# Kernel optimization log

Measured on AMD Instinct MI355X. Metric: run time of the kernel, lower is better.

The kernel has to match this reference:

```python
import jax, jax.numpy as jnp
import numpy as np

B, T, IN, H = 128, 128, 64, 512  # batch, seq_len, input_size, encoded_size==hidden_size


def _cell(x, h, c, Wih, Whh, bih, bhh):
    # PyTorch LSTM gate order: i, f, g, o
    g = x @ Wih.T + h @ Whh.T + bih + bhh
    i, f, gg, o = jnp.split(g, 4, axis=-1)
    c = jax.nn.sigmoid(f) * c + jax.nn.sigmoid(i) * jnp.tanh(gg)
    h = jax.nn.sigmoid(o) * jnp.tanh(c)
    return h, c


def _lstm_layer(xs, Wih, Whh, bih, bhh):
    # xs: [T, B, din] -> ys: [T, B, H], zero initial state (as in the torch module)
    b = xs.shape[1]
    hdim = Whh.shape[1]
    h0 = jnp.zeros((b, hdim), xs.dtype)
    c0 = jnp.zeros((b, hdim), xs.dtype)

    def step(carry, x):
        h, c = _cell(x, carry[0], carry[1], Wih, Whh, bih, bhh)
        return (h, c), h

    _, ys = jax.lax.scan(step, (h0, c0), xs)
    return ys


def setup_inputs() -> dict:
    key = jax.random.key(0)
    ks = jax.random.split(key, 18)
    s = 1.0 / np.sqrt(H)  # torch LSTM default init scale
    r = lambda k, shp: jax.random.uniform(k, shp, jnp.float32, -s, s)
    return {
        "x": jax.random.normal(ks[0], (B, T, IN), jnp.float32),
        # encoder layer 0 (input IN) and layer 1 (input H)
        "eW_ih0": r(ks[1], (4 * H, IN)), "eW_hh0": r(ks[2], (4 * H, H)),
        "eb_ih0": r(ks[3], (4 * H,)), "eb_hh0": r(ks[4], (4 * H,)),
        "eW_ih1": r(ks[5], (4 * H, H)), "eW_hh1": r(ks[6], (4 * H, H)),
        "eb_ih1": r(ks[7], (4 * H,)), "eb_hh1": r(ks[8], (4 * H,)),
        # decoder layer 0 (input H = encoded_size) and layer 1
        "dW_ih0": r(ks[9], (4 * H, H)), "dW_hh0": r(ks[10], (4 * H, H)),
        "db_ih0": r(ks[11], (4 * H,)), "db_hh0": r(ks[12], (4 * H,)),
        "dW_ih1": r(ks[13], (4 * H, H)), "dW_hh1": r(ks[14], (4 * H, H)),
        "db_ih1": r(ks[15], (4 * H,)), "db_hh1": r(ks[16], (4 * H,)),
        # output projection
        "fc_W": r(ks[17], (IN, H)), "fc_b": jnp.zeros((IN,), jnp.float32),
    }


def reference(x, eW_ih0, eW_hh0, eb_ih0, eb_hh0, eW_ih1, eW_hh1, eb_ih1, eb_hh1,
              dW_ih0, dW_hh0, db_ih0, db_hh0, dW_ih1, dW_hh1, db_ih1, db_hh1,
              fc_W, fc_b):
    b, t = x.shape[0], x.shape[1]
    xs = jnp.swapaxes(x, 0, 1)  # [T, B, IN]
    # 2-layer encoder, take last timestep of top layer
    y0 = _lstm_layer(xs, eW_ih0, eW_hh0, eb_ih0, eb_hh0)
    y1 = _lstm_layer(y0, eW_ih1, eW_hh1, eb_ih1, eb_hh1)
    z = y1[-1]  # [B, H] constant decoder input each step
    hdim = dW_hh0.shape[1]
    zero = jnp.zeros((b, hdim), x.dtype)

    def step(carry, _):
        h0, c0, h1, c1 = carry
        h0, c0 = _cell(z, h0, c0, dW_ih0, dW_hh0, db_ih0, db_hh0)
        h1, c1 = _cell(h0, h1, c1, dW_ih1, dW_hh1, db_ih1, db_hh1)
        return (h0, c0, h1, c1), h1

    _, hs = jax.lax.scan(step, (zero, zero, zero, zero), None, length=t)  # [T, B, H]
    out = jnp.einsum('tbh,ih->tbi', hs, fc_W) + fc_b
    return jnp.swapaxes(out, 0, 1)  # [B, T, IN]
```

## Files before the change

### kernel.cpp

```cpp
#include <hip/hip_runtime.h>
#include <cstdint>

#define TT 128

typedef _Float16 f16;
typedef _Float16 f16x8 __attribute__((ext_vector_type(8)));
typedef float f32x4 __attribute__((ext_vector_type(4)));
typedef unsigned int u32;
typedef unsigned long long u64;

#define OFF_H0    16384
#define OFF_H1    (OFF_H0 + 262144)
#define OFF_D0    (OFF_H1 + 262144)
#define OFF_D1    (OFF_D0 + 262144)
#define OFF_XH    (OFF_D1 + 262144)
#define OFF_HS    (OFF_XH + 2097152)

#define L_SA   0
#define L_SB   24576
#define L_TOT  65536

#define MFMA16(a,b,c) __builtin_amdgcn_mfma_f32_16x16x32_f16((a),(b),(c),0,0,0)

__device__ __forceinline__ float sigm(float x){ return 1.f/(1.f+__expf(-x)); }
__device__ __forceinline__ float tanhft(float x){ return 1.f - 2.f/(__expf(2.f*x)+1.f); }

__device__ __forceinline__ f16x8 wfrag(const float* __restrict__ src, int K, int srow,
                                       int k, int j){
  const float* p = src + srow*K + (k<<5) + (j<<3);
  float4 v0 = *(const float4*)p;
  float4 v1 = *(const float4*)(p+4);
  f16x8 r;
  r[0]=(f16)v0.x; r[1]=(f16)v0.y; r[2]=(f16)v0.z; r[3]=(f16)v0.w;
  r[4]=(f16)v1.x; r[5]=(f16)v1.y; r[6]=(f16)v1.z; r[7]=(f16)v1.w;
  return r;
}

__device__ __forceinline__ void stage1(const char* R, char* S, int tid){
  const int cgs = tid >> 3, rr = (tid & 7) << 1;
  const char* gp = R + cgs*512 + rr*32;
  char* sp = S + cgs*768 + rr*48;
  u64 t0[8];
#pragma unroll
  for (int e = 0; e < 2; ++e)
#pragma unroll
    for (int i = 0; i < 4; ++i)
      t0[e*4+i] = __hip_atomic_load((const u64*)(gp + e*32 + i*8),
                                    __ATOMIC_RELAXED, __HIP_MEMORY_SCOPE_AGENT);
#pragma unroll
  for (int e = 0; e < 2; ++e)
#pragma unroll
    for (int i = 0; i < 4; ++i)
      *(u64*)(sp + e*48 + i*8) = t0[e*4+i];
}

__device__ __forceinline__ void stage2(const char* R0, const char* R1,
                                       char* SA, char* SB, int tid){
  const int cgs = tid >> 3, rr = (tid & 7) << 1;
  const char* g0 = R0 + cgs*512 + rr*32;
  const char* g1 = R1 + cgs*512 + rr*32;
  char* s0 = SA + cgs*768 + rr*48;
  char* s1 = SB + cgs*768 + rr*48;
  u64 t0[8], t1[8];
#pragma unroll
  for (int e = 0; e < 2; ++e)
#pragma unroll
    for (int i = 0; i < 4; ++i)
      t0[e*4+i] = __hip_atomic_load((const u64*)(g0 + e*32 + i*8),
                                    __ATOMIC_RELAXED, __HIP_MEMORY_SCOPE_AGENT);
#pragma unroll
  for (int e = 0; e < 2; ++e)
#pragma unroll
    for (int i = 0; i < 4; ++i)
      t1[e*4+i] = __hip_atomic_load((const u64*)(g1 + e*32 + i*8),
                                    __ATOMIC_RELAXED, __HIP_MEMORY_SCOPE_AGENT);
#pragma unroll
  for (int e = 0; e < 2; ++e)
#pragma unroll
    for (int i = 0; i < 4; ++i)
      *(u64*)(s0 + e*48 + i*8) = t0[e*4+i];
#pragma unroll
  for (int e = 0; e < 2; ++e)
#pragma unroll
    for (int i = 0; i < 4; ++i)
      *(u64*)(s1 + e*48 + i*8) = t1[e*4+i];
}

__device__ __forceinline__ void gbar(int* fl, int g, int cg, int tid, int target){
  __syncthreads();
  if (tid == 0)
    __hip_atomic_store(&fl[((g<<5)+cg)<<4], target,
                       __ATOMIC_RELAXED, __HIP_MEMORY_SCOPE_AGENT);
  if (tid < 64){
    int idx = ((g<<5) + (tid & 31)) << 4;
    bool ok = __hip_atomic_load(&fl[idx], __ATOMIC_RELAXED, __HIP_MEMORY_SCOPE_AGENT) >= target;
    while (!__all(ok)){
      __builtin_amdgcn_s_sleep(1);
      ok = __hip_atomic_load(&fl[idx], __ATOMIC_RELAXED, __HIP_MEMORY_SCOPE_AGENT) >= target;
    }
  }
  __syncthreads();
}

__global__ void cvt_x(const float* __restrict__ x, char* __restrict__ ws){
  int i = blockIdx.x*256 + threadIdx.x;
  int p = i & 3, b = (i >> 2) & 127, t = i >> 9;
  const float* s = x + (((b<<7) + t)<<6) + (p<<4);
  float4 v0 = *(const float4*)s,     v1 = *(const float4*)(s+4);
  float4 v2 = *(const float4*)(s+8), v3 = *(const float4*)(s+12);
  f16x8 h0, h1;
  h0[0]=(f16)v0.x; h0[1]=(f16)v0.y; h0[2]=(f16)v0.z; h0[3]=(f16)v0.w;
  h0[4]=(f16)v1.x; h0[5]=(f16)v1.y; h0[6]=(f16)v1.z; h0[7]=(f16)v1.w;
  h1[0]=(f16)v2.x; h1[1]=(f16)v2.y; h1[2]=(f16)v2.z; h1[3]=(f16)v2.w;
  h1[4]=(f16)v3.x; h1[5]=(f16)v3.y; h1[6]=(f16)v3.z; h1[7]=(f16)v3.w;
  char* d = ws + OFF_XH + ((((t<<3) + (b>>4))<<4) + (b&15))*128 + (p<<5);
  *(f16x8*)d = h0;
  *(f16x8*)(d+16) = h1;
}

__global__ __launch_bounds__(256, 1) void lstm_persist(
    const float* __restrict__ eWih0, const float* __restrict__ eWhh0,
    const float* __restrict__ ebi0,  const float* __restrict__ ebh0,
    const float* __restrict__ eWih1, const float* __restrict__ eWhh1,
    const float* __restrict__ ebi1,  const float* __restrict__ ebh1,
    const float* __restrict__ dWih0, const float* __restrict__ dWhh0,
    const float* __restrict__ dbi0,  const float* __restrict__ dbh0,
    const float* __restrict__ dWih1, const float* __restrict__ dWhh1,
    const float* __restrict__ dbi1,  const float* __restrict__ dbh1,
    const float* __restrict__ fcW,   const float* __restrict__ fcb,
    float* __restrict__ out, char* __restrict__ ws)
{
  __shared__ __align__(16) char lds[L_TOT];
  const int tid  = threadIdx.x;
  const int wg   = blockIdx.x;
  const int g    = wg & 7;
  const int cg   = wg >> 3;
  const int b0   = g << 4;
  const int lane = tid & 63, w = tid >> 6;
  const int j    = lane >> 4;
  const int arow = lane & 15;
  const int bq   = lane & 15;
  const int srow = ((bq&3)<<9) + (cg<<4) + (w<<2) + (bq>>2);
  const int lq   = lane & 3;
  const int hcc  = (lane >> 2) & 3;
  const int row_c = ((lane>>4)<<2) + lq;

  int* flags = (int*)ws;
  char* H0 = ws + OFF_H0;  char* H1 = ws + OFF_H1;
  char* D0 = ws + OFF_D0;  char* D1 = ws + OFF_D1;
  const char* XH = ws + OFF_XH;
  char* HS = ws + OFF_HS;
  char* SA = lds + L_SA; char* SB = lds + L_SB;

  const int abase = ((j>>1)*768) + arow*48 + ((j&1)<<4);
  const int hst = cg*512 + row_c*32 + (w<<3);

  f16x8 wA[16], wB[16], wC[16], wX0, wX1;
#pragma unroll
  for (int k = 0; k < 16; ++k){
    wA[k] = wfrag(eWhh0, 512, srow, k, j);
    wB[k] = wfrag(eWih1, 512, srow, k, j);
    wC[k] = wfrag(eWhh1, 512, srow, k, j);
  }
  wX0 = wfrag(eWih0, 64, srow, 0, j);
  wX1 = wfrag(eWih0, 64, srow, 1, j);
  float B0r[4], B1r[4];
#pragma unroll
  for (int e = 0; e < 4; ++e){
    int bi = (e<<9) + (cg<<4) + (w<<2) + hcc;
    B0r[e] = ebi0[bi] + ebh0[bi];
    B1r[e] = ebi1[bi] + ebh1[bi];
  }

  auto qtr = [&](f32x4 a) -> f32x4 {
    float s0 = __shfl_xor(a[1],1), s1 = __shfl_xor(a[0],1);
    float s2 = __shfl_xor(a[3],1), s3 = __shfl_xor(a[2],1);
    bool o1 = lane & 1;
    float c0 = o1 ? s0 : a[0];
    float c1 = o1 ? a[1] : s1;
    float c2 = o1 ? s2 : a[2];
    float c3 = o1 ? a[3] : s3;
    float u0 = __shfl_xor(c2,2), u1 = __shfl_xor(c3,2);
    float u2 = __shfl_xor(c0,2), u3 = __shfl_xor(c1,2);
    bool o2 = lane & 2;
    f32x4 t;
    t[0] = o2 ? u0 : c0;
    t[1] = o2 ? u1 : c1;
    t[2] = o2 ? c2 : u2;
    t[3] = o2 ? c3 : u3;
    return t;
  };

  float c0v = 0.f, c1v = 0.f;
  int bt = 0;

  for (int s = 0; s <= TT; ++s){
    const bool d0 = (s < TT), d1 = (s >= 1);
    const char* R0 = H0 + (((s&1)<<3) + g)*16384;
    const char* R1 = H1 + (((s&1)<<3) + g)*16384;
    char* W0 = H0 + ((((s+1)&1)<<3) + g)*16384;
    char* W1 = H1 + ((((s+1)&1)<<3) + g)*16384;

    stage2(R0, R1, SA, SB, tid);
    f16x8 xa0, xa1;
    if (d0){
      const char* xg = XH + (((s<<3) + g)<<11) + arow*128 + (j<<4);
      xa0 = *(const f16x8*)(xg);
      xa1 = *(const f16x8*)(xg + 64);
    }
    __syncthreads();

    f32x4 acc0 = {0.f,0.f,0.f,0.f}, acc1 = {0.f,0.f,0.f,0.f};
    if (d0){
      acc0 = MFMA16(xa0, wX0, acc0);
      acc0 = MFMA16(xa1, wX1, acc0);
    }
#pragma unroll
    for (int k = 0; k < 16; ++k){
      f16x8 a0 = *(const f16x8*)(SA + k*1536 + abase);
      f16x8 a1 = *(const f16x8*)(SB + k*1536 + abase);
      acc0 = MFMA16(a0, wA[k], acc0);
      acc1 = MFMA16(a0, wB[k], acc1);
      acc1 = MFMA16(a1, wC[k], acc1);
    }

    if (d0){
      f32x4 t = qtr(acc0);
      float gi = sigm(t[0]+B0r[0]), gf = sigm(t[1]+B0r[1]);
      float gg = tanhft(t[2]+B0r[2]), go = sigm(t[3]+B0r[3]);
      c0v = gf*c0v + gi*gg;
      float h = go * tanhft(c0v);
      union { f16 hf; unsigned short su; } cv; cv.hf = (f16)h;
      u32 v = cv.su;
      u32 p = v | (((u32)(unsigned short)__shfl_xor((int)v, 4)) << 16);
      u32 q = (u32)__shfl_xor((int)p, 8);
      if (!(lane & 12)){
        u64 pk = (u64)p | ((u64)q << 32);
        __hip_atomic_store((u64*)(W0 + hst), pk,
                           __ATOMIC_RELAXED, __HIP_MEMORY_SCOPE_AGENT);
      }
    }
    if (d1){
      f32x4 t = qtr(acc1);
      float gi = sigm(t[0]+B1r[0]), gf = sigm(t[1]+B1r[1]);
      float gg = tanhft(t[2]+B1r[2]), go = sigm(t[3]+B1r[3]);
      c1v = gf*c1v + gi*gg;
      float h = go * tanhft(c1v);
      union { f16 hf; unsigned short su; } cv; cv.hf = (f16)h;
      u32 v = cv.su;
      u32 p = v | (((u32)(unsigned short)__shfl_xor((int)v, 4)) << 16);
      u32 q = (u32)__shfl_xor((int)p, 8);
      if (!(lane & 12)){
        u64 pk = (u64)p | ((u64)q << 32);
        __hip_atomic_store((u64*)(W1 + hst), pk,
                           __ATOMIC_RELAXED, __HIP_MEMORY_SCOPE_AGENT);
      }
    }
    gbar(flags, g, cg, tid, ++bt);
  }

  f32x4 zx;
  {
    stage1(H1 + (8 + g)*16384, SA, tid);
    f16x8 wZ[16];
#pragma unroll
    for (int k = 0; k < 16; ++k) wZ[k] = wfrag(dWih0, 512, srow, k, j);
    float zb = dbi0[srow] + dbh0[srow];
    zx[0]=zb; zx[1]=zb; zx[2]=zb; zx[3]=zb;
    __syncthreads();
#pragma unroll
    for (int k = 0; k < 16; ++k)
      zx = MFMA16(*(const f16x8*)(SA + k*1536 + abase), wZ[k], zx);
  }

#pragma unroll
  for (int k = 0; k < 16; ++k){
    wA[k] = wfrag(dWhh0, 512, srow, k, j);
    wB[k] = wfrag(dWih1, 512, srow, k, j);
    wC[k] = wfrag(dWhh1, 512, srow, k, j);
  }
#pragma unroll
  for (int e = 0; e < 4; ++e){
    int bi = (e<<9) + (cg<<4) + (w<<2) + hcc;
    B1r[e] = dbi1[bi] + dbh1[bi];
  }
  c0v = 0.f; c1v = 0.f;

  for (int s = 0; s <= TT; ++s){
    const bool d0 = (s < TT), d1 = (s >= 1);
    const char* R0 = D0 + (((s&1)<<3) + g)*16384;
    const char* R1 = D1 + (((s&1)<<3) + g)*16384;
    char* W0 = D0 + ((((s+1)&1)<<3) + g)*16384;
    char* W1 = D1 + ((((s+1)&1)<<3) + g)*16384;

    stage2(R0, R1, SA, SB, tid);
    __syncthreads();

    f32x4 acc0 = zx, acc1 = {0.f,0.f,0.f,0.f};
#pragma unroll
    for (int k = 0; k < 16; ++k){
      f16x8 a0 = *(const f16x8*)(SA + k*1536 + abase);
      f16x8 a1 = *(const f16x8*)(SB + k*1536 + abase);
      acc0 = MFMA16(a0, wA[k], acc0);
      acc1 = MFMA16(a0, wB[k], acc1);
      acc1 = MFMA16(a1, wC[k], acc1);
    }

    if (d0){
      f32x4 t = qtr(acc0);
      float gi = sigm(t[0]), gf = sigm(t[1]);
      float gg = tanhft(t[2]), go = sigm(t[3]);
      c0v = gf*c0v + gi*gg;
      float h = go * tanhft(c0v);
      union { f16 hf; unsigned short su; } cv; cv.hf = (f16)h;
      u32 v = cv.su;
      u32 p = v | (((u32)(unsigned short)__shfl_xor((int)v, 4)) << 16);
      u32 q = (u32)__shfl_xor((int)p, 8);
      if (!(lane & 12)){
        u64 pk = (u64)p | ((u64)q << 32);
        __hip_atomic_store((u64*)(W0 + hst), pk,
                           __ATOMIC_RELAXED, __HIP_MEMORY_SCOPE_AGENT);
      }
    }
    if (d1){
      f32x4 t = qtr(acc1);
      float gi = sigm(t[0]+B1r[0]), gf = sigm(t[1]+B1r[1]);
      float gg = tanhft(t[2]+B1r[2]), go = sigm(t[3]+B1r[3]);
      c1v = gf*c1v + gi*gg;
      float h = go * tanhft(c1v);
      union { f16 hf; unsigned short su; } cv; cv.hf = (f16)h;
      u32 v = cv.su;
      u32 p = v | (((u32)(unsigned short)__shfl_xor((int)v, 4)) << 16);
      u32 q = (u32)__shfl_xor((int)p, 8);
      if (!(lane & 12)){
        u64 pk = (u64)p | ((u64)q << 32);
        __hip_atomic_store((u64*)(W1 + hst), pk,
                           __ATOMIC_RELAXED, __HIP_MEMORY_SCOPE_AGENT);
        __hip_atomic_store((u64*)(HS + (((s-1)<<7) + b0 + row_c)*1024 + cg*32 + (w<<3)), pk,
                           __ATOMIC_RELAXED, __HIP_MEMORY_SCOPE_AGENT);
      }
    }
    gbar(flags, g, cg, tid, ++bt);
  }

  __builtin_amdgcn_fence(__ATOMIC_ACQUIRE, "agent");
  __syncthreads();

  for (int qd = tid; qd < 8192; qd += 256){
    int i = qd >> 7, kq = qd & 127;
    float4 v = *(const float4*)(fcW + (i<<9) + (kq<<2));
    f16* p = (f16*)(lds + (i<<10) + (kq<<3));
    p[0]=(f16)v.x; p[1]=(f16)v.y; p[2]=(f16)v.z; p[3]=(f16)v.w;
  }
  __syncthreads();
  {
    int t  = (cg<<2) + w;
    int r  = (lane >> 2) & 15;
    int iq = lane & 3;
    const char* hsrow = HS + (((t<<7) + b0 + r)<<10);
    float acc[16];
#pragma unroll
    for (int ii = 0; ii < 16; ++ii) acc[ii] = 0.f;
    for (int k8 = 0; k8 < 64; ++k8){
      f16x8 hv = *(const f16x8*)(hsrow + (k8<<4));
#pragma unroll
      for (int ii = 0; ii < 16; ++ii){
        f16x8 wv = *(const f16x8*)(lds + (((iq<<4)+ii)<<10) + (k8<<4));
#pragma unroll
        for (int jj = 0; jj < 8; ++jj) acc[ii] += (float)hv[jj] * (float)wv[jj];
      }
    }
#pragma unroll
    for (int ii = 0; ii < 16; ++ii){
      int i = (iq<<4) + ii;
      out[((((b0+r)<<7) + t)<<6) + i] = acc[ii] + fcb[i];
    }
  }
}

extern "C" void kernel_launch(void* const* d_in, const int* in_sizes, int n_in,
                              void* d_out, int out_size, void* d_ws, size_t ws_size,
                              hipStream_t stream){
  const float* x     = (const float*)d_in[0];
  const float* eWih0 = (const float*)d_in[1];
  const float* eWhh0 = (const float*)d_in[2];
  const float* ebi0  = (const float*)d_in[3];
  const float* ebh0  = (const float*)d_in[4];
  const float* eWih1 = (const float*)d_in[5];
  const float* eWhh1 = (const float*)d_in[6];
  const float* ebi1  = (const float*)d_in[7];
  const float* ebh1  = (const float*)d_in[8];
  const float* dWih0 = (const float*)d_in[9];
  const float* dWhh0 = (const float*)d_in[10];
  const float* dbi0  = (const float*)d_in[11];
  const float* dbh0  = (const float*)d_in[12];
  const float* dWih1 = (const float*)d_in[13];
  const float* dWhh1 = (const float*)d_in[14];
  const float* dbi1  = (const float*)d_in[15];
  const float* dbh1  = (const float*)d_in[16];
  const float* fcW   = (const float*)d_in[17];
  const float* fcb   = (const float*)d_in[18];
  char* ws = (char*)d_ws;

  hipMemsetAsync(d_ws, 0, OFF_XH, stream);
  cvt_x<<<256, 256, 0, stream>>>(x, ws);
  lstm_persist<<<256, 256, 0, stream>>>(eWih0,eWhh0,ebi0,ebh0,eWih1,eWhh1,ebi1,ebh1,
                                        dWih0,dWhh0,dbi0,dbh0,dWih1,dWhh1,dbi1,dbh1,
                                        fcW,fcb,(float*)d_out,ws);
}
```

Before: 1.533 ms.

## Replace per-block flag barrier with atomic counter barrier and pin weight registers

The group barrier changes from per-workgroup flag slots polled by a full wavefront to a single per-group counter. Each block increments it with fetch_add and one thread spins until the count reaches 32 times the step. Weight fragments and biases are pinned in VGPRs with empty asm so the compiler cannot rematerialize or reload them inside the loop. The counter barrier reduces the polling work per block, but all 32 blocks now contend on one cache line.

```diff
diff --git a/kernel.cpp b/kernel.cpp
--- a/kernel.cpp
+++ b/kernel.cpp
@@ -8,6 +8,8 @@
 typedef float f32x4 __attribute__((ext_vector_type(4)));
 typedef unsigned int u32;
 typedef unsigned long long u64;
+
+#define PIN(v) asm volatile("" : "+v"(v))
 
 #define OFF_H0    16384
 #define OFF_H1    (OFF_H0 + 262144)
@@ -86,17 +88,13 @@
       *(u64*)(s1 + e*48 + i*8) = t1[e*4+i];
 }
 
-__device__ __forceinline__ void gbar(int* fl, int g, int cg, int tid, int target){
+__device__ __forceinline__ void gbar(u32* cnt, int tid, u32 target32){
   __syncthreads();
-  if (tid == 0)
-    __hip_atomic_store(&fl[((g<<5)+cg)<<4], target,
-                       __ATOMIC_RELAXED, __HIP_MEMORY_SCOPE_AGENT);
-  if (tid < 64){
-    int idx = ((g<<5) + (tid & 31)) << 4;
-    bool ok = __hip_atomic_load(&fl[idx], __ATOMIC_RELAXED, __HIP_MEMORY_SCOPE_AGENT) >= target;
-    while (!__all(ok)){
+  if (tid == 0){
+    u32 c = __hip_atomic_fetch_add(cnt, 1, __ATOMIC_RELAXED, __HIP_MEMORY_SCOPE_AGENT) + 1;
+    while (c < target32){
       __builtin_amdgcn_s_sleep(1);
-      ok = __hip_atomic_load(&fl[idx], __ATOMIC_RELAXED, __HIP_MEMORY_SCOPE_AGENT) >= target;
+      c = __hip_atomic_load(cnt, __ATOMIC_RELAXED, __HIP_MEMORY_SCOPE_AGENT);
     }
   }
   __syncthreads();
@@ -145,12 +143,12 @@
   const int hcc  = (lane >> 2) & 3;
   const int row_c = ((lane>>4)<<2) + lq;
 
-  int* flags = (int*)ws;
+  u32* cnt = (u32*)(ws + (g<<6));
   char* H0 = ws + OFF_H0;  char* H1 = ws + OFF_H1;
   char* D0 = ws + OFF_D0;  char* D1 = ws + OFF_D1;
   const char* XH = ws + OFF_XH;
   char* HS = ws + OFF_HS;
-  char* SA = lds + L_SA; char* SB = lds + L_SB;
+  char* SA = lds + 0; char* SB = lds + L_SB;
 
   const int abase = ((j>>1)*768) + arow*48 + ((j&1)<<4);
   const int hst = cg*512 + row_c*32 + (w<<3);
@@ -158,18 +156,18 @@
   f16x8 wA[16], wB[16], wC[16], wX0, wX1;
 #pragma unroll
   for (int k = 0; k < 16; ++k){
-    wA[k] = wfrag(eWhh0, 512, srow, k, j);
-    wB[k] = wfrag(eWih1, 512, srow, k, j);
-    wC[k] = wfrag(eWhh1, 512, srow, k, j);
-  }
-  wX0 = wfrag(eWih0, 64, srow, 0, j);
-  wX1 = wfrag(eWih0, 64, srow, 1, j);
+    wA[k] = wfrag(eWhh0, 512, srow, k, j);  PIN(wA[k]);
+    wB[k] = wfrag(eWih1, 512, srow, k, j);  PIN(wB[k]);
+    wC[k] = wfrag(eWhh1, 512, srow, k, j);  PIN(wC[k]);
+  }
+  wX0 = wfrag(eWih0, 64, srow, 0, j);  PIN(wX0);
+  wX1 = wfrag(eWih0, 64, srow, 1, j);  PIN(wX1);
   float B0r[4], B1r[4];
 #pragma unroll
   for (int e = 0; e < 4; ++e){
     int bi = (e<<9) + (cg<<4) + (w<<2) + hcc;
-    B0r[e] = ebi0[bi] + ebh0[bi];
-    B1r[e] = ebi1[bi] + ebh1[bi];
+    B0r[e] = ebi0[bi] + ebh0[bi];  PIN(B0r[e]);
+    B1r[e] = ebi1[bi] + ebh1[bi];  PIN(B1r[e]);
   }
 
   auto qtr = [&](f32x4 a) -> f32x4 {
@@ -192,7 +190,7 @@
   };
 
   float c0v = 0.f, c1v = 0.f;
-  int bt = 0;
+  u32 bt = 0;
 
   for (int s = 0; s <= TT; ++s){
     const bool d0 = (s < TT), d1 = (s >= 1);
@@ -256,7 +254,7 @@
                            __ATOMIC_RELAXED, __HIP_MEMORY_SCOPE_AGENT);
       }
     }
-    gbar(flags, g, cg, tid, ++bt);
+    gbar(cnt, tid, (++bt) << 5);
   }
 
   f32x4 zx;
@@ -275,14 +273,14 @@
 
 #pragma unroll
   for (int k = 0; k < 16; ++k){
-    wA[k] = wfrag(dWhh0, 512, srow, k, j);
-    wB[k] = wfrag(dWih1, 512, srow, k, j);
-    wC[k] = wfrag(dWhh1, 512, srow, k, j);
+    wA[k] = wfrag(dWhh0, 512, srow, k, j);  PIN(wA[k]);
+    wB[k] = wfrag(dWih1, 512, srow, k, j);  PIN(wB[k]);
+    wC[k] = wfrag(dWhh1, 512, srow, k, j);  PIN(wC[k]);
   }
 #pragma unroll
   for (int e = 0; e < 4; ++e){
     int bi = (e<<9) + (cg<<4) + (w<<2) + hcc;
-    B1r[e] = dbi1[bi] + dbh1[bi];
+    B1r[e] = dbi1[bi] + dbh1[bi];  PIN(B1r[e]);
   }
   c0v = 0.f; c1v = 0.f;
 
@@ -340,7 +338,7 @@
                            __ATOMIC_RELAXED, __HIP_MEMORY_SCOPE_AGENT);
       }
     }
-    gbar(flags, g, cg, tid, ++bt);
+    gbar(cnt, tid, (++bt) << 5);
   }
 
   __builtin_amdgcn_fence(__ATOMIC_ACQUIRE, "agent");
```

Result: faster. 1.386 ms (-9.5%).
